# Kernel optimization log

Hardware: AMD Instinct MI355X
Metric: run time of the kernel (lower is better)

The kernel has to match this reference:

```python
import jax, jax.numpy as jnp
import numpy as np

N_NODES = 100000
N_EDGES = 1600000
IN_CH = 128
HID = 64
OUT_CH = 16
N_GRAPHS = 512
NEG_SLOPE = 0.2


def setup_inputs() -> dict:
    key = jax.random.key(0)
    ks = jax.random.split(key, 24)
    x = jax.random.normal(ks[0], (N_NODES, IN_CH), dtype=jnp.float32)
    edge_index = jax.random.randint(ks[1], (2, N_EDGES), 0, N_NODES, dtype=jnp.int64)
    batch = jnp.sort(jax.random.randint(ks[2], (N_NODES,), 0, N_GRAPHS, dtype=jnp.int64))
    s = 0.05
    p = {
        'W_l1': jax.random.normal(ks[3], (IN_CH, HID)) * s,
        'b_l1': jnp.zeros((HID,), jnp.float32),
        'W_r1': jax.random.normal(ks[4], (IN_CH, HID)) * s,
        'b_r1': jnp.zeros((HID,), jnp.float32),
        'att1': jax.random.normal(ks[5], (HID,)) * s,
        'bias1': jnp.zeros((HID,), jnp.float32),
        'W_l2': jax.random.normal(ks[6], (HID, HID)) * s,
        'b_l2': jnp.zeros((HID,), jnp.float32),
        'W_r2': jax.random.normal(ks[7], (HID, HID)) * s,
        'b_r2': jnp.zeros((HID,), jnp.float32),
        'att2': jax.random.normal(ks[8], (HID,)) * s,
        'bias2': jnp.zeros((HID,), jnp.float32),
        'W_fc1': jax.random.normal(ks[9], (HID, HID)) * s,
        'b_fc1': jnp.zeros((HID,), jnp.float32),
        'gamma': jnp.ones((HID,), jnp.float32),
        'beta': jnp.zeros((HID,), jnp.float32),
        'W_fc2': jax.random.normal(ks[10], (HID, OUT_CH)) * s,
        'b_fc2': jnp.zeros((OUT_CH,), jnp.float32),
    }
    return dict(x=x, edge_index=edge_index, batch=batch, **p)


def _gatv2_layer(x, src, dst, Wl, bl, Wr, br, att, bias):
    # GATv2Conv (heads=1): x_l = lin_l(x), x_r = lin_r(x)
    xl = x @ Wl + bl              # [N, H] source transform
    xr = x @ Wr + br              # [N, H] target transform
    # per-edge score: att . LeakyReLU(x_l[j] + x_r[i])
    h = xl[src] + xr[dst]         # [E, H]
    h = jnp.where(h >= 0, h, NEG_SLOPE * h)
    e = h @ att                   # [E]
    # scatter-softmax over incoming edges of each target node
    m = jax.ops.segment_max(e, dst, num_segments=N_NODES)
    a = jnp.exp(e - m[dst])
    z = jax.ops.segment_sum(a, dst, num_segments=N_NODES)
    alpha = a / z[dst]            # every node has a self-loop -> z > 0
    out = jax.ops.segment_sum(alpha[:, None] * xl[src], dst, num_segments=N_NODES)
    return out + bias


def reference(x, edge_index, batch, W_l1, b_l1, W_r1, b_r1, att1, bias1,
              W_l2, b_l2, W_r2, b_r2, att2, bias2,
              W_fc1, b_fc1, gamma, beta, W_fc2, b_fc2):
    loop = jnp.arange(N_NODES, dtype=edge_index.dtype)
    src = jnp.concatenate([edge_index[0], loop])  # add_self_loops=True
    dst = jnp.concatenate([edge_index[1], loop])
    h = _gatv2_layer(x, src, dst, W_l1, b_l1, W_r1, b_r1, att1, bias1)
    h = jax.nn.relu(h)
    h = _gatv2_layer(h, src, dst, W_l2, b_l2, W_r2, b_r2, att2, bias2)
    # global mean pool over graphs
    sums = jax.ops.segment_sum(h, batch, num_segments=N_GRAPHS)
    cnt = jax.ops.segment_sum(jnp.ones((N_NODES,), h.dtype), batch, num_segments=N_GRAPHS)
    g = sums / jnp.clip(cnt, 1.0)[:, None]        # [G, H]
    # MLP head: Linear -> BatchNorm1d (training-mode batch stats) -> ReLU -> Linear
    y = g @ W_fc1 + b_fc1
    mu = jnp.mean(y, axis=0)
    var = jnp.var(y, axis=0)
    y = gamma * (y - mu) * jax.lax.rsqrt(var + 1e-5) + beta
    y = jax.nn.relu(y)
    y = y @ W_fc2 + b_fc2
    return jax.nn.log_softmax(y, axis=1)
```

## Files before the change

kernel.cpp:

```cpp
#include <hip/hip_runtime.h>

#define N_NODES 100000
#define N_EDGES 1600000
#define IN_CH 128
#define HID 64
#define OUT_CH 16
#define N_GRAPHS 512
#define NEG_SLOPE 0.2f

#define MAX_DEG 64

#define GEMM1_BLOCKS ((N_NODES + 127) / 128)
#define DEG_EPT 8
#define DEG_BLOCKS ((N_EDGES + 256 * DEG_EPT - 1) / (256 * DEG_EPT))
#define FUSED_BLOCKS (GEMM1_BLOCKS + DEG_BLOCKS)

#define NEG_BIG (-1e30f)
#define LDSP 132

typedef float f32x2 __attribute__((ext_vector_type(2)));

__device__ __forceinline__ f32x2 pkmax(f32x2 a, f32x2 b) {
  return __builtin_elementwise_max(a, b);
}
__device__ __forceinline__ f32x2 pkfma(f32x2 a, f32x2 b, f32x2 c) {
  return __builtin_elementwise_fma(a, b, c);
}

__device__ __forceinline__ unsigned int f2bf_pack(float lo, float hi) {
  unsigned int ul = __float_as_uint(lo);
  unsigned int uh = __float_as_uint(hi);
  ul = (ul + 0x7FFFu + ((ul >> 16) & 1u)) >> 16;
  uh = (uh + 0x7FFFu + ((uh >> 16) & 1u)) >> 16;
  return ul | (uh << 16);
}
__device__ __forceinline__ float bf2f(unsigned short b) {
  return __uint_as_float(((unsigned int)b) << 16);
}

__device__ __forceinline__ int deg_alloc(unsigned int* degp, int d) {
  unsigned int sh = (d & 3) * 8;
  unsigned int old = atomicAdd(&degp[d >> 2], 1u << sh);
  return (int)((old >> sh) & 255u);
}
__device__ __forceinline__ int deg_read(const unsigned int* degp, int d) {
  return (int)((degp[d >> 2] >> ((d & 3) * 8)) & 255u);
}


__global__ __launch_bounds__(256) void k_fused_gemm1_scatter(
    const float* __restrict__ x,
    const float* __restrict__ Wl, const float* __restrict__ bl,
    const float* __restrict__ Wr, const float* __restrict__ br,
    unsigned short* __restrict__ xlb, unsigned short* __restrict__ xrb,
    const int* __restrict__ src, const int* __restrict__ dst,
    unsigned int* __restrict__ deg, int* __restrict__ adjP) {
  constexpr int K = IN_CH;
  constexpr int KC = 16;
  constexpr int NCH = K / KC;
  __shared__ float xs[KC][LDSP];
  __shared__ float ws[KC][LDSP];

  int b = blockIdx.x;
  if (b & 1) {
    int db = b >> 1;
    int base = (db * 256 + threadIdx.x) * DEG_EPT;
    if (base + DEG_EPT <= N_EDGES) {
      int4 d4a = *(const int4*)&dst[base];
      int4 d4b = *(const int4*)&dst[base + 4];
      int4 s4a = *(const int4*)&src[base];
      int4 s4b = *(const int4*)&src[base + 4];
      int d[8] = {d4a.x, d4a.y, d4a.z, d4a.w, d4b.x, d4b.y, d4b.z, d4b.w};
      int s[8] = {s4a.x, s4a.y, s4a.z, s4a.w, s4b.x, s4b.y, s4b.z, s4b.w};
      int sl[8];
      #pragma unroll
      for (int u = 0; u < 8; u++) sl[u] = deg_alloc(deg, d[u]);
      #pragma unroll
      for (int u = 0; u < 8; u++)
        if (sl[u] < MAX_DEG) adjP[d[u] * MAX_DEG + sl[u]] = s[u];
    } else {
      for (int e = base; e < N_EDGES; e++) {
        int dd = dst[e];
        int sl = deg_alloc(deg, dd);
        if (sl < MAX_DEG) adjP[dd * MAX_DEG + sl] = src[e];
      }
    }
    return;
  }

  int tid = threadIdx.x;
  int tx = tid & 15;
  int ty = tid >> 4;
  int nb = (b >> 1) * 128;

  float acc[8][8];
  #pragma unroll
  for (int i = 0; i < 8; i++)
    #pragma unroll
    for (int j = 0; j < 8; j++) acc[i][j] = 0.f;

  for (int c = 0; c < NCH; c++) {
    int kc = c * KC;
    if (c) __syncthreads();
    #pragma unroll
    for (int j = 0; j < 2; j++) {
      int idx = tid + 256 * j;
      int node = idx >> 2, q = idx & 3;
      int gn = nb + node;
      float4 v = make_float4(0.f, 0.f, 0.f, 0.f);
      if (gn < N_NODES) v = *(const float4*)&x[(size_t)gn * K + kc + q * 4];
      xs[q * 4 + 0][node] = v.x;
      xs[q * 4 + 1][node] = v.y;
      xs[q * 4 + 2][node] = v.z;
      xs[q * 4 + 3][node] = v.w;
    }
    #pragma unroll
    for (int j = 0; j < 2; j++) {
      int idx = tid + 256 * j;
      int k = idx >> 5, cc = idx & 31;
      float4 v;
      if (cc < 16) v = *(const float4*)&Wl[(size_t)(kc + k) * 64 + cc * 4];
      else         v = *(const float4*)&Wr[(size_t)(kc + k) * 64 + (cc - 16) * 4];
      *(float4*)&ws[k][cc * 4] = v;
    }
    __syncthreads();

    #pragma unroll 4
    for (int k = 0; k < KC; k++) {
      float4 a0 = *(const float4*)&xs[k][ty * 8];
      float4 a1 = *(const float4*)&xs[k][ty * 8 + 4];
      float4 b0 = *(const float4*)&ws[k][tx * 8];
      float4 b1 = *(const float4*)&ws[k][tx * 8 + 4];
      float av[8] = {a0.x, a0.y, a0.z, a0.w, a1.x, a1.y, a1.z, a1.w};
      float bv[8] = {b0.x, b0.y, b0.z, b0.w, b1.x, b1.y, b1.z, b1.w};
      #pragma unroll
      for (int i = 0; i < 8; i++)
        #pragma unroll
        for (int j = 0; j < 8; j++)
          acc[i][j] = fmaf(av[i], bv[j], acc[i][j]);
    }
  }

  int f0 = tx * 8;
  float bb[8];
  #pragma unroll
  for (int j = 0; j < 8; j++)
    bb[j] = (f0 < 64) ? bl[f0 + j] : br[f0 - 64 + j];
  unsigned short* outp = (f0 < 64) ? xlb : xrb;
  int fo = (f0 < 64) ? f0 : f0 - 64;
  #pragma unroll
  for (int i = 0; i < 8; i++) {
    int node = nb + ty * 8 + i;
    if (node < N_NODES) {
      int4 o;
      o.x = (int)f2bf_pack(acc[i][0] + bb[0], acc[i][1] + bb[1]);
      o.y = (int)f2bf_pack(acc[i][2] + bb[2], acc[i][3] + bb[3]);
      o.z = (int)f2bf_pack(acc[i][4] + bb[4], acc[i][5] + bb[5]);
      o.w = (int)f2bf_pack(acc[i][6] + bb[6], acc[i][7] + bb[7]);
      *(int4*)&outp[(size_t)node * 64 + fo] = o;
    }
  }
}


template <int K>
__global__ __launch_bounds__(256) void k_dual_gemm(
    const float* __restrict__ x,
    const float* __restrict__ Wl, const float* __restrict__ bl,
    const float* __restrict__ Wr, const float* __restrict__ br,
    unsigned short* __restrict__ xlb, unsigned short* __restrict__ xrb) {
  constexpr int KC = 32;
  constexpr int NCH = K / KC;
  __shared__ float xs[KC][LDSP];
  __shared__ float ws[KC][LDSP];

  int tid = threadIdx.x;
  int tx = tid & 15;
  int ty = tid >> 4;
  int nb = blockIdx.x * 128;

  float acc[8][8];
  #pragma unroll
  for (int i = 0; i < 8; i++)
    #pragma unroll
    for (int j = 0; j < 8; j++) acc[i][j] = 0.f;

  for (int c = 0; c < NCH; c++) {
    int kc = c * KC;
    if (c) __syncthreads();
    #pragma unroll
    for (int j = 0; j < 4; j++) {
      int idx = tid + 256 * j;
      int node = idx >> 3, q = idx & 7;
      int gn = nb + node;
      float4 v = make_float4(0.f, 0.f, 0.f, 0.f);
      if (gn < N_NODES) v = *(const float4*)&x[(size_t)gn * K + kc + q * 4];
      xs[q * 4 + 0][node] = v.x;
      xs[q * 4 + 1][node] = v.y;
      xs[q * 4 + 2][node] = v.z;
      xs[q * 4 + 3][node] = v.w;
    }
    #pragma unroll
    for (int j = 0; j < 4; j++) {
      int idx = tid + 256 * j;
      int k = idx >> 5, cc = idx & 31;
      float4 v;
      if (cc < 16) v = *(const float4*)&Wl[(size_t)(kc + k) * 64 + cc * 4];
      else         v = *(const float4*)&Wr[(size_t)(kc + k) * 64 + (cc - 16) * 4];
      *(float4*)&ws[k][cc * 4] = v;
    }
    __syncthreads();

    #pragma unroll 4
    for (int k = 0; k < KC; k++) {
      float4 a0 = *(const float4*)&xs[k][ty * 8];
      float4 a1 = *(const float4*)&xs[k][ty * 8 + 4];
      float4 b0 = *(const float4*)&ws[k][tx * 8];
      float4 b1 = *(const float4*)&ws[k][tx * 8 + 4];
      float av[8] = {a0.x, a0.y, a0.z, a0.w, a1.x, a1.y, a1.z, a1.w};
      float bv[8] = {b0.x, b0.y, b0.z, b0.w, b1.x, b1.y, b1.z, b1.w};
      #pragma unroll
      for (int i = 0; i < 8; i++)
        #pragma unroll
        for (int j = 0; j < 8; j++)
          acc[i][j] = fmaf(av[i], bv[j], acc[i][j]);
    }
  }

  int f0 = tx * 8;
  float bb[8];
  #pragma unroll
  for (int j = 0; j < 8; j++)
    bb[j] = (f0 < 64) ? bl[f0 + j] : br[f0 - 64 + j];
  unsigned short* outp = (f0 < 64) ? xlb : xrb;
  int fo = (f0 < 64) ? f0 : f0 - 64;
  #pragma unroll
  for (int i = 0; i < 8; i++) {
    int node = nb + ty * 8 + i;
    if (node < N_NODES) {
      int4 o;
      o.x = (int)f2bf_pack(acc[i][0] + bb[0], acc[i][1] + bb[1]);
      o.y = (int)f2bf_pack(acc[i][2] + bb[2], acc[i][3] + bb[3]);
      o.z = (int)f2bf_pack(acc[i][4] + bb[4], acc[i][5] + bb[5]);
      o.w = (int)f2bf_pack(acc[i][6] + bb[6], acc[i][7] + bb[7]);
      *(int4*)&outp[(size_t)node * 64 + fo] = o;
    }
  }
}


__global__ __launch_bounds__(256) void k_gat(
    const unsigned short* __restrict__ xlb, const unsigned short* __restrict__ xrb,
    const float* __restrict__ att, const float* __restrict__ bias,
    const unsigned int* __restrict__ deg, const int* __restrict__ adjP,
    float* __restrict__ out, int do_relu) {
  int wid = (blockIdx.x * 256 + threadIdx.x) >> 6;
  int lane = threadIdx.x & 63;
  if (wid >= N_NODES) return;
  int fg = lane & 15;
  int sub = lane >> 4;

  int degv = deg_read(deg, wid);
  degv = (degv < MAX_DEG) ? degv : MAX_DEG;
  int L = degv + 1;

  int eidx = wid;
  if (lane < degv) eidx = adjP[(size_t)wid * MAX_DEG + lane];

  ushort4 xrr = *(const ushort4*)&xrb[(size_t)wid * 64 + fg * 4];
  f32x2 xr01 = {bf2f(xrr.x), bf2f(xrr.y)};
  f32x2 xr23 = {bf2f(xrr.z), bf2f(xrr.w)};
  float4 att4 = *(const float4*)&att[fg * 4];
  f32x2 at01 = {att4.x, att4.y};
  f32x2 at23 = {att4.z, att4.w};
  const f32x2 ns = {NEG_SLOPE, NEG_SLOPE};

  float z = 0.f;
  f32x2 acc01 = {0.f, 0.f};
  f32x2 acc23 = {0.f, 0.f};

  for (int p0 = 0; p0 < L; p0 += 8) {
    int q0 = p0 + sub * 2;
    int q1 = q0 + 1;
    bool act0 = (q0 < L);
    bool act1 = (q1 < L);
    int sj0 = __shfl(eidx, (q0 - 1) & 63, 64);
    int sj1 = __shfl(eidx, (q1 - 1) & 63, 64);
    int j0 = (q0 == 0) ? wid : sj0;
    int j1 = sj1;
    ushort4 raw0 = make_ushort4(0, 0, 0, 0);
    ushort4 raw1 = make_ushort4(0, 0, 0, 0);
    if (act0) raw0 = *(const ushort4*)&xlb[(size_t)j0 * 64 + fg * 4];
    if (act1) raw1 = *(const ushort4*)&xlb[(size_t)j1 * 64 + fg * 4];
    f32x2 v0a = {bf2f(raw0.x), bf2f(raw0.y)};
    f32x2 v0b = {bf2f(raw0.z), bf2f(raw0.w)};
    f32x2 v1a = {bf2f(raw1.x), bf2f(raw1.y)};
    f32x2 v1b = {bf2f(raw1.z), bf2f(raw1.w)};

    f32x2 a0 = v0a + xr01, b0 = v0b + xr23;
    a0 = pkmax(a0, a0 * ns);
    b0 = pkmax(b0, b0 * ns);
    f32x2 s0v = pkfma(a0, at01, b0 * at23);
    float s0 = s0v.x + s0v.y;

    f32x2 a1 = v1a + xr01, b1 = v1b + xr23;
    a1 = pkmax(a1, a1 * ns);
    b1 = pkmax(b1, b1 * ns);
    f32x2 s1v = pkfma(a1, at01, b1 * at23);
    float s1 = s1v.x + s1v.y;

    #pragma unroll
    for (int o = 1; o <= 8; o <<= 1) {
      s0 += __shfl_xor(s0, o, 64);
      s1 += __shfl_xor(s1, o, 64);
    }

    float w0 = act0 ? __expf(s0) : 0.f;
    float w1 = act1 ? __expf(s1) : 0.f;
    z += w0 + w1;
    f32x2 w0v = {w0, w0};
    f32x2 w1v = {w1, w1};
    acc01 = pkfma(w0v, v0a, pkfma(w1v, v1a, acc01));
    acc23 = pkfma(w0v, v0b, pkfma(w1v, v1b, acc23));
  }

  #pragma unroll
  for (int o = 16; o <= 32; o <<= 1) {
    z += __shfl_xor(z, o, 64);
    acc01.x += __shfl_xor(acc01.x, o, 64);
    acc01.y += __shfl_xor(acc01.y, o, 64);
    acc23.x += __shfl_xor(acc23.x, o, 64);
    acc23.y += __shfl_xor(acc23.y, o, 64);
  }

  if (sub == 0) {
    float4 b4 = *(const float4*)&bias[fg * 4];
    float inv = 1.f / z;
    float4 r;
    r.x = acc01.x * inv + b4.x;
    r.y = acc01.y * inv + b4.y;
    r.z = acc23.x * inv + b4.z;
    r.w = acc23.y * inv + b4.w;
    if (do_relu) {
      r.x = fmaxf(r.x, 0.f); r.y = fmaxf(r.y, 0.f);
      r.z = fmaxf(r.z, 0.f); r.w = fmaxf(r.w, 0.f);
    }
    *(float4*)&out[(size_t)wid * 64 + fg * 4] = r;
  }
}


__device__ __forceinline__ int lower_bound_batch(const int* __restrict__ b, int key) {
  int lo = 0, hi = N_NODES;
  while (lo < hi) {
    int mid = (lo + hi) >> 1;
    if (b[mid] < key) lo = mid + 1; else hi = mid;
  }
  return lo;
}

__global__ void k_pool_head1(const float* __restrict__ h, const int* __restrict__ batch,
                             const float* __restrict__ W, const float* __restrict__ b,
                             float* __restrict__ y) {
  __shared__ int s_range[2];
  __shared__ float red[256];
  __shared__ float gm[64];
  int g = blockIdx.x, t = threadIdx.x;
  if (t == 0) s_range[0] = lower_bound_batch(batch, g);
  if (t == 1) s_range[1] = lower_bound_batch(batch, g + 1);
  __syncthreads();
  int lo = s_range[0], hi = s_range[1];
  int f = t & 63, sub = t >> 6;
  float acc = 0.f;
  for (int n = lo + sub; n < hi; n += 4) acc += h[n * 64 + f];
  red[t] = acc;
  __syncthreads();
  if (sub == 0) {
    float s = red[f] + red[64 + f] + red[128 + f] + red[192 + f];
    int cnt = hi - lo;
    if (cnt < 1) cnt = 1;
    gm[f] = s / (float)cnt;
  }
  __syncthreads();
  float a2 = 0.f;
  #pragma unroll 4
  for (int k = sub * 16; k < sub * 16 + 16; k++) a2 = fmaf(gm[k], W[k * 64 + f], a2);
  red[t] = a2;
  __syncthreads();
  if (sub == 0)
    y[g * 64 + f] = b[f] + red[f] + red[64 + f] + red[128 + f] + red[192 + f];
}


__global__ void k_bnstats(const float* __restrict__ y, float* __restrict__ mu,
                          float* __restrict__ rstd) {
  __shared__ float rs[256], rss[256];
  int f = blockIdx.x, t = threadIdx.x;
  float v0 = y[t * 64 + f];
  float v1 = y[(t + 256) * 64 + f];
  rs[t] = v0 + v1;
  rss[t] = v0 * v0 + v1 * v1;
  __syncthreads();
  #pragma unroll
  for (int o = 128; o > 0; o >>= 1) {
    if (t < o) { rs[t] += rs[t + o]; rss[t] += rss[t + o]; }
    __syncthreads();
  }
  if (t == 0) {
    float m = rs[0] / (float)N_GRAPHS;
    float var = rss[0] / (float)N_GRAPHS - m * m;
    mu[f] = m;
    rstd[f] = rsqrtf(var + 1e-5f);
  }
}

__global__ void k_head2(const float* __restrict__ y, const float* __restrict__ gamma,
                        const float* __restrict__ beta, const float* __restrict__ mu,
                        const float* __restrict__ rstd, const float* __restrict__ W2,
                        const float* __restrict__ b2, float* __restrict__ out) {
  int idx = blockIdx.x * 256 + threadIdx.x;
  if (idx >= N_GRAPHS * OUT_CH) return;
  int gi = idx >> 4, o = idx & 15;
  float acc = b2[o];
  #pragma unroll
  for (int k = 0; k < 64; k++) {
    float v = y[gi * 64 + k];
    v = gamma[k] * (v - mu[k]) * rstd[k] + beta[k];
    v = fmaxf(v, 0.f);
    acc = fmaf(v, W2[k * OUT_CH + o], acc);
  }
  float mx = acc;
  #pragma unroll
  for (int w = 8; w > 0; w >>= 1) mx = fmaxf(mx, __shfl_xor(mx, w, 16));
  float ex = __expf(acc - mx);
  float s = ex;
  #pragma unroll
  for (int w = 8; w > 0; w >>= 1) s += __shfl_xor(s, w, 16);
  out[idx] = acc - mx - __logf(s);
}


extern "C" void kernel_launch(void* const* d_in, const int* in_sizes, int n_in,
                              void* d_out, int out_size, void* d_ws, size_t ws_size,
                              hipStream_t stream) {
  const float* x      = (const float*)d_in[0];
  const int*   edge   = (const int*)d_in[1];
  const int*   batch  = (const int*)d_in[2];
  const float* W_l1   = (const float*)d_in[3];
  const float* b_l1   = (const float*)d_in[4];
  const float* W_r1   = (const float*)d_in[5];
  const float* b_r1   = (const float*)d_in[6];
  const float* att1   = (const float*)d_in[7];
  const float* bias1  = (const float*)d_in[8];
  const float* W_l2   = (const float*)d_in[9];
  const float* b_l2   = (const float*)d_in[10];
  const float* W_r2   = (const float*)d_in[11];
  const float* b_r2   = (const float*)d_in[12];
  const float* att2   = (const float*)d_in[13];
  const float* bias2  = (const float*)d_in[14];
  const float* W_fc1  = (const float*)d_in[15];
  const float* b_fc1  = (const float*)d_in[16];
  const float* gamma  = (const float*)d_in[17];
  const float* beta   = (const float*)d_in[18];
  const float* W_fc2  = (const float*)d_in[19];
  const float* b_fc2  = (const float*)d_in[20];

  const int* src = edge;
  const int* dst = edge + N_EDGES;

  char* ws = (char*)d_ws;
  size_t off = 0;
  auto alloc = [&](size_t bytes) -> void* {
    off = (off + 255) & ~(size_t)255;
    void* p = ws + off;
    off += bytes;
    return p;
  };
  unsigned int* deg = (unsigned int*)alloc(((size_t)N_NODES / 4 + 4) * 4);
  int* adjP     = (int*)alloc((size_t)N_NODES * MAX_DEG * 4);
  unsigned short* xlb = (unsigned short*)alloc((size_t)N_NODES * HID * 2);
  unsigned short* xrb = (unsigned short*)alloc((size_t)N_NODES * HID * 2);
  float* h      = (float*)alloc((size_t)N_NODES * HID * 4);
  float* y      = (float*)alloc((size_t)N_GRAPHS * HID * 4);
  float* mu     = (float*)alloc(64 * 4);
  float* rstd   = (float*)alloc(64 * 4);

  hipMemsetAsync(deg, 0, ((size_t)N_NODES / 4 + 4) * 4, stream);

  k_fused_gemm1_scatter<<<FUSED_BLOCKS, 256, 0, stream>>>(
      x, W_l1, b_l1, W_r1, b_r1, xlb, xrb, src, dst, deg, adjP);

  k_gat<<<(N_NODES + 3) / 4, 256, 0, stream>>>(xlb, xrb, att1, bias1, deg, adjP, h, 1);
  k_dual_gemm<HID><<<(N_NODES + 127) / 128, 256, 0, stream>>>(h, W_l2, b_l2, W_r2, b_r2, xlb, xrb);
  k_gat<<<(N_NODES + 3) / 4, 256, 0, stream>>>(xlb, xrb, att2, bias2, deg, adjP, h, 0);

  k_pool_head1<<<N_GRAPHS, 256, 0, stream>>>(h, batch, W_fc1, b_fc1, y);
  k_bnstats<<<64, 256, 0, stream>>>(y, mu, rstd);
  k_head2<<<(N_GRAPHS * OUT_CH + 255) / 256, 256, 0, stream>>>(y, gamma, beta, mu, rstd,
                                                               W_fc2, b_fc2, (float*)d_out);
}
```

Baseline: 391.0 us.

## Fuse pooling, batchnorm stats and head into one cooperative kernel

```diff
diff --git a/kernel.cpp b/kernel.cpp
--- a/kernel.cpp
+++ b/kernel.cpp
@@ -1,4 +1,5 @@
 #include <hip/hip_runtime.h>
+#include <hip/hip_cooperative_groups.h>
 
 #define N_NODES 100000
 #define N_EDGES 1600000
@@ -359,84 +360,91 @@
   return lo;
 }
 
-__global__ void k_pool_head1(const float* __restrict__ h, const int* __restrict__ batch,
-                             const float* __restrict__ W, const float* __restrict__ b,
-                             float* __restrict__ y) {
+__global__ void k_tail(const float* __restrict__ h, const int* __restrict__ batch,
+                       const float* __restrict__ W1, const float* __restrict__ b1,
+                       const float* __restrict__ gamma, const float* __restrict__ beta,
+                       const float* __restrict__ W2, const float* __restrict__ b2,
+                       float* __restrict__ y, float* __restrict__ mu,
+                       float* __restrict__ rstd, float* __restrict__ out) {
   __shared__ int s_range[2];
   __shared__ float red[256];
+  __shared__ float red2[256];
   __shared__ float gm[64];
-  int g = blockIdx.x, t = threadIdx.x;
-  if (t == 0) s_range[0] = lower_bound_batch(batch, g);
-  if (t == 1) s_range[1] = lower_bound_batch(batch, g + 1);
-  __syncthreads();
-  int lo = s_range[0], hi = s_range[1];
-  int f = t & 63, sub = t >> 6;
-  float acc = 0.f;
-  for (int n = lo + sub; n < hi; n += 4) acc += h[n * 64 + f];
-  red[t] = acc;
-  __syncthreads();
-  if (sub == 0) {
-    float s = red[f] + red[64 + f] + red[128 + f] + red[192 + f];
-    int cnt = hi - lo;
-    if (cnt < 1) cnt = 1;
-    gm[f] = s / (float)cnt;
-  }
-  __syncthreads();
-  float a2 = 0.f;
-  #pragma unroll 4
-  for (int k = sub * 16; k < sub * 16 + 16; k++) a2 = fmaf(gm[k], W[k * 64 + f], a2);
-  red[t] = a2;
-  __syncthreads();
-  if (sub == 0)
-    y[g * 64 + f] = b[f] + red[f] + red[64 + f] + red[128 + f] + red[192 + f];
-}
-
-
-__global__ void k_bnstats(const float* __restrict__ y, float* __restrict__ mu,
-                          float* __restrict__ rstd) {
-  __shared__ float rs[256], rss[256];
-  int f = blockIdx.x, t = threadIdx.x;
-  float v0 = y[t * 64 + f];
-  float v1 = y[(t + 256) * 64 + f];
-  rs[t] = v0 + v1;
-  rss[t] = v0 * v0 + v1 * v1;
-  __syncthreads();
-  #pragma unroll
-  for (int o = 128; o > 0; o >>= 1) {
-    if (t < o) { rs[t] += rs[t + o]; rss[t] += rss[t + o]; }
-    __syncthreads();
-  }
-  if (t == 0) {
-    float m = rs[0] / (float)N_GRAPHS;
-    float var = rss[0] / (float)N_GRAPHS - m * m;
-    mu[f] = m;
-    rstd[f] = rsqrtf(var + 1e-5f);
-  }
-}
-
-__global__ void k_head2(const float* __restrict__ y, const float* __restrict__ gamma,
-                        const float* __restrict__ beta, const float* __restrict__ mu,
-                        const float* __restrict__ rstd, const float* __restrict__ W2,
-                        const float* __restrict__ b2, float* __restrict__ out) {
-  int idx = blockIdx.x * 256 + threadIdx.x;
-  if (idx >= N_GRAPHS * OUT_CH) return;
-  int gi = idx >> 4, o = idx & 15;
-  float acc = b2[o];
-  #pragma unroll
-  for (int k = 0; k < 64; k++) {
-    float v = y[gi * 64 + k];
-    v = gamma[k] * (v - mu[k]) * rstd[k] + beta[k];
-    v = fmaxf(v, 0.f);
-    acc = fmaf(v, W2[k * OUT_CH + o], acc);
-  }
-  float mx = acc;
-  #pragma unroll
-  for (int w = 8; w > 0; w >>= 1) mx = fmaxf(mx, __shfl_xor(mx, w, 16));
-  float ex = __expf(acc - mx);
-  float s = ex;
-  #pragma unroll
-  for (int w = 8; w > 0; w >>= 1) s += __shfl_xor(s, w, 16);
-  out[idx] = acc - mx - __logf(s);
+  int t = threadIdx.x;
+
+  {
+    int g = blockIdx.x;
+    if (t == 0) s_range[0] = lower_bound_batch(batch, g);
+    if (t == 1) s_range[1] = lower_bound_batch(batch, g + 1);
+    __syncthreads();
+    int lo = s_range[0], hi = s_range[1];
+    int f = t & 63, sub = t >> 6;
+    float acc = 0.f;
+    for (int n = lo + sub; n < hi; n += 4) acc += h[n * 64 + f];
+    red[t] = acc;
+    __syncthreads();
+    if (sub == 0) {
+      float s = red[f] + red[64 + f] + red[128 + f] + red[192 + f];
+      int cnt = hi - lo;
+      if (cnt < 1) cnt = 1;
+      gm[f] = s / (float)cnt;
+    }
+    __syncthreads();
+    float a2 = 0.f;
+    #pragma unroll 4
+    for (int k = sub * 16; k < sub * 16 + 16; k++) a2 = fmaf(gm[k], W1[k * 64 + f], a2);
+    red[t] = a2;
+    __syncthreads();
+    if (sub == 0)
+      y[g * 64 + f] = b1[f] + red[f] + red[64 + f] + red[128 + f] + red[192 + f];
+  }
+
+  cooperative_groups::this_grid().sync();
+
+  if (blockIdx.x < 64) {
+    int f = blockIdx.x;
+    float v0 = y[t * 64 + f];
+    float v1 = y[(t + 256) * 64 + f];
+    red[t] = v0 + v1;
+    red2[t] = v0 * v0 + v1 * v1;
+    __syncthreads();
+    #pragma unroll
+    for (int o = 128; o > 0; o >>= 1) {
+      if (t < o) { red[t] += red[t + o]; red2[t] += red2[t + o]; }
+      __syncthreads();
+    }
+    if (t == 0) {
+      float m = red[0] / (float)N_GRAPHS;
+      float var = red2[0] / (float)N_GRAPHS - m * m;
+      mu[f] = m;
+      rstd[f] = rsqrtf(var + 1e-5f);
+    }
+  }
+
+  cooperative_groups::this_grid().sync();
+
+  if (blockIdx.x < 32) {
+    int idx = blockIdx.x * 256 + t;
+    if (idx < N_GRAPHS * OUT_CH) {
+      int gi = idx >> 4, o = idx & 15;
+      float acc = b2[o];
+      #pragma unroll
+      for (int k = 0; k < 64; k++) {
+        float v = y[gi * 64 + k];
+        v = gamma[k] * (v - mu[k]) * rstd[k] + beta[k];
+        v = fmaxf(v, 0.f);
+        acc = fmaf(v, W2[k * OUT_CH + o], acc);
+      }
+      float mx = acc;
+      #pragma unroll
+      for (int w = 8; w > 0; w >>= 1) mx = fmaxf(mx, __shfl_xor(mx, w, 16));
+      float ex = __expf(acc - mx);
+      float s = ex;
+      #pragma unroll
+      for (int w = 8; w > 0; w >>= 1) s += __shfl_xor(s, w, 16);
+      out[idx] = acc - mx - __logf(s);
+    }
+  }
 }
 
 
@@ -494,8 +502,9 @@
   k_dual_gemm<HID><<<(N_NODES + 127) / 128, 256, 0, stream>>>(h, W_l2, b_l2, W_r2, b_r2, xlb, xrb);
   k_gat<<<(N_NODES + 3) / 4, 256, 0, stream>>>(xlb, xrb, att2, bias2, deg, adjP, h, 0);
 
-  k_pool_head1<<<N_GRAPHS, 256, 0, stream>>>(h, batch, W_fc1, b_fc1, y);
-  k_bnstats<<<64, 256, 0, stream>>>(y, mu, rstd);
-  k_head2<<<(N_GRAPHS * OUT_CH + 255) / 256, 256, 0, stream>>>(y, gamma, beta, mu, rstd,
-                                                               W_fc2, b_fc2, (float*)d_out);
-}
+  float* outp = (float*)d_out;
+  void* args[] = {(void*)&h, (void*)&batch, (void*)&W_fc1, (void*)&b_fc1,
+                  (void*)&gamma, (void*)&beta, (void*)&W_fc2, (void*)&b_fc2,
+                  (void*)&y, (void*)&mu, (void*)&rstd, (void*)&outp};
+  hipLaunchCooperativeKernel((void*)k_tail, dim3(N_GRAPHS), dim3(256), args, 0, stream);
+}
```

Measured after the change: 538.2 us. +37.7%, slower.
